# Kernel optimization log

Hardware: AMD Instinct MI355X
Metric: run time of the kernel (lower is better)

Reference implementation:

```python
import jax, jax.numpy as jnp
import numpy as np

B, CTX, QST, E, H = 8, 4096, 512, 300, 128

def setup_inputs() -> dict:
    key = jax.random.key(0)
    k1, k2, k3, k4 = jax.random.split(key, 4)
    context_sequence = jax.random.normal(k1, (B, CTX, E), dtype=jnp.float32)
    question_sequence = jax.random.normal(k2, (B, QST, E), dtype=jnp.float32)
    question_mask = jnp.ones((B, QST), dtype=jnp.int32)
    # dense layer params (PyTorch Linear: y = x @ W.T + b)
    bound = 1.0 / np.sqrt(E)
    W = jax.random.uniform(k3, (H, E), minval=-bound, maxval=bound, dtype=jnp.float32)
    b = jax.random.uniform(k4, (H,), minval=-bound, maxval=bound, dtype=jnp.float32)
    return {"context_sequence": context_sequence, "question_sequence": question_sequence,
            "question_mask": question_mask, "W": W, "b": b}

def reference(context_sequence, question_sequence, question_mask, W, b):
    # ReLU(dense(x)) for both sequences
    ctx_logits = jax.nn.relu(jnp.einsum('bce,he->bch', context_sequence, W) + b)   # [B, CTX, H]
    qst_logits = jax.nn.relu(jnp.einsum('bqe,he->bqh', question_sequence, W) + b)  # [B, QST, H]
    scores = jnp.einsum('bch,bqh->bcq', ctx_logits, qst_logits)                    # [B, CTX, QST]
    scores = jnp.where(question_mask[:, None, :] == 0, -jnp.inf, scores)
    attn = jax.nn.softmax(scores, axis=-1)
    return jnp.einsum('bcq,bqh->bch', attn, qst_logits)                            # [B, CTX, H]
```

## Files before the change

kernel.cpp:

```cpp
#include <hip/hip_runtime.h>
#include <hip/hip_bf16.h>

#define BB   8
#define SCTX 4096
#define SQ   512
#define EE   300
#define HH   128
#define EP   320
#define CST  328
#define QCH  136
#define LOG2E 1.4426950408889634f

typedef short bhalf4 __attribute__((ext_vector_type(4)));
typedef short short8 __attribute__((ext_vector_type(8)));
typedef float f32x4  __attribute__((ext_vector_type(4)));
typedef unsigned u32x4 __attribute__((ext_vector_type(4)));

#define MFMA16(a, b, c) __builtin_amdgcn_mfma_f32_16x16x32_bf16((a), (b), (c), 0, 0, 0)

__device__ __forceinline__ short f2bf(float f) {
  unsigned u = __builtin_bit_cast(unsigned, f);
  u += 0x7fffu + ((u >> 16) & 1u);
  return (short)(u >> 16);
}
__device__ __forceinline__ float bf2f(short s) {
  return __builtin_bit_cast(float, ((unsigned)(unsigned short)s) << 16);
}
__device__ __forceinline__ unsigned pack2(float a, float b) {
  return (unsigned)(unsigned short)f2bf(a) | ((unsigned)(unsigned short)f2bf(b) << 16);
}

__global__ void k_wpad(const float* __restrict__ W, short* __restrict__ wsw) {
  const int h = blockIdx.x, k = threadIdx.x;
  float v = (k < EE) ? W[h * EE + k] : 0.0f;
  const int m = h >> 4, t = h & 15, kk = k >> 5, quad = (k >> 3) & 3, j = k & 7;
  wsw[((kk * 8 + m) * 64 + quad * 16 + t) * 8 + j] = f2bf(v);
}

__global__ __launch_bounds__(256) void k_qlog(const float* __restrict__ qst,
                                              const short* __restrict__ wsw,
                                              const float* __restrict__ bias,
                                              short* __restrict__ ql,
                                              short* __restrict__ qlT) {
  const int b = blockIdx.y;
  const int m0 = blockIdx.x * 32;
  const int tid = threadIdx.x;
  const int w = tid >> 6, l = tid & 63, t = l & 15, quad = l >> 4;
  const int g = w >> 1, hf = w & 1;

  __shared__ __align__(16) short cst[32 * CST];

  const float4* cbase = (const float4*)(qst + (size_t)(b * SQ + m0) * EE);
#pragma unroll
  for (int j = 0; j < 10; ++j) {
    int i4 = tid + j * 256;
    if (i4 < 2400) {
      float4 v = cbase[i4];
      int row = i4 / 75, c4 = i4 - row * 75;
      short* dp = cst + row * CST + c4 * 4;
      dp[0] = f2bf(v.x); dp[1] = f2bf(v.y); dp[2] = f2bf(v.z); dp[3] = f2bf(v.w);
    }
  }
  for (int i = tid; i < 320; i += 256) {
    int row = i / 10, c = (i - row * 10) * 2;
    cst[row * CST + 300 + c] = 0;
    cst[row * CST + 301 + c] = 0;
  }
  __syncthreads();

  const short* arow = cst + (g * 16 + t) * CST;
  f32x4 acc[4] = {};
#pragma unroll
  for (int kk = 0; kk < 10; ++kk) {
    const int k = kk * 32 + quad * 8;
    short8 a = *(const short8*)(arow + k);
#pragma unroll
    for (int n = 0; n < 4; ++n) {
      short8 w8 = *(const short8*)(wsw + ((kk * 8 + hf * 4 + n) * 64 + l) * 8);
      acc[n] = MFMA16(a, w8, acc[n]);
    }
  }
#pragma unroll
  for (int n = 0; n < 4; ++n) {
    const int h = (hf * 4 + n) * 16 + t;
    const float bv = bias[h];
#pragma unroll
    for (int r = 0; r < 4; ++r) {
      float v = fmaxf(acc[n][r] + bv, 0.0f);
      short s16 = f2bf(v);
      const int row = m0 + g * 16 + quad * 4 + r;
      ql[((size_t)b * SQ + row) * HH + h] = s16;
      qlT[((size_t)b * HH + h) * SQ + row] = s16;
    }
  }
}

__global__ __launch_bounds__(256, 2) void k_attn(const float* __restrict__ ctx,
                                                 const short* __restrict__ wsw,
                                                 const float* __restrict__ bias,
                                                 const int* __restrict__ mask,
                                                 const short* __restrict__ ql,
                                                 const short* __restrict__ qlT,
                                                 float* __restrict__ out) {
  const int b = blockIdx.y;
  const int m0 = blockIdx.x * 64;
  const int tid = threadIdx.x;
  const int w = tid >> 6, l = tid & 63, t = l & 15, quad = l >> 4;
  const int g = w >> 1, hf = w & 1;

  __shared__ __align__(16) short uq[17408];
  __shared__ __align__(16) short uv[17408];
  __shared__ short maskh[SQ];
  short* cst = uq;
  short* qch = uq;
  short* clt = uv;
  short* vch = uv;

  const short8* qsrc = (const short8*)(ql + (size_t)b * SQ * HH);
  const short8* vsrc = (const short8*)(qlT + (size_t)b * HH * SQ);

  short8 qreg[8], vreg[8];
#pragma unroll
  for (int j = 0; j < 8; ++j) {
    int i = tid + j * 256;
    qreg[j] = qsrc[i];
    vreg[j] = vsrc[(i >> 4) * 64 + (i & 15)];
  }

  for (int i = tid; i < SQ; i += 256)
    maskh[i] = f2bf(mask[b * SQ + i] ? -8.0f : -1e30f);

  for (int i = 0; i < 2; ++i) {
    const float4* cbase = (const float4*)(ctx + ((size_t)b * SCTX + m0 + i * 32) * EE);
#pragma unroll
    for (int j = 0; j < 10; ++j) {
      int i4 = tid + j * 256;
      if (i4 < 2400) {
        float4 v = cbase[i4];
        int row = i4 / 75, c4 = i4 - row * 75;
        short* dp = cst + row * CST + c4 * 4;
        dp[0] = f2bf(v.x); dp[1] = f2bf(v.y); dp[2] = f2bf(v.z); dp[3] = f2bf(v.w);
      }
    }
    for (int k = tid; k < 320; k += 256) {
      int row = k / 10, c = (k - row * 10) * 2;
      cst[row * CST + 300 + c] = 0;
      cst[row * CST + 301 + c] = 0;
    }
    __syncthreads();
    const short* arow = cst + (g * 16 + t) * CST;
    f32x4 acc[4] = {};
#pragma unroll
    for (int kk = 0; kk < 10; ++kk) {
      const int k = kk * 32 + quad * 8;
      short8 a = *(const short8*)(arow + k);
#pragma unroll
      for (int n = 0; n < 4; ++n) {
        short8 w8 = *(const short8*)(wsw + ((kk * 8 + hf * 4 + n) * 64 + l) * 8);
        acc[n] = MFMA16(a, w8, acc[n]);
      }
    }
#pragma unroll
    for (int n = 0; n < 4; ++n) {
      const int h = (hf * 4 + n) * 16 + t;
      const float bv = bias[h];
#pragma unroll
      for (int r = 0; r < 4; ++r) {
        float v = fmaxf(acc[n][r] + bv, 0.0f);
        clt[(i * 32 + g * 16 + quad * 4 + r) * 136 + h] = f2bf(v);
      }
    }
    __syncthreads();
  }

  short8 af[4];
#pragma unroll
  for (int kk = 0; kk < 4; ++kk)
    af[kk] = *(const short8*)&clt[(w * 16 + t) * 136 + kk * 32 + quad * 8];
  __syncthreads();

#pragma unroll
  for (int j = 0; j < 8; ++j) {
    int i = tid + j * 256;
    *(short8*)&qch[(i >> 4) * QCH + (i & 15) * 8] = qreg[j];
    *(short8*)&vch[(i >> 4) * QCH + (i & 15) * 8] = vreg[j];
  }

  const int srcA = ((quad & 1) * 2) * 16 + t;
  const int srcB = srcA + 16;
  const bool hiq = quad >= 2;

  f32x4 o[8] = {};
  float rtot = 0.0f;
  for (int c = 0; c < 4; ++c) {
    __syncthreads();
    if (c < 3) {
#pragma unroll
      for (int j = 0; j < 8; ++j) {
        int i = tid + j * 256;
        qreg[j] = qsrc[(c + 1) * 2048 + i];
        vreg[j] = vsrc[(i >> 4) * 64 + (c + 1) * 16 + (i & 15)];
      }
    }
#pragma unroll
    for (int kk = 0; kk < 4; ++kk) {
      f32x4 svE = {0.f, 0.f, 0.f, 0.f}, svO = {0.f, 0.f, 0.f, 0.f};
      const short* qrE = qch + ((kk * 2) * 16 + t) * QCH;
      const short* qrO = qch + ((kk * 2 + 1) * 16 + t) * QCH;
#pragma unroll
      for (int kx = 0; kx < 4; ++kx) {
        short8 b8e = *(const short8*)(qrE + kx * 32 + quad * 8);
        short8 b8o = *(const short8*)(qrO + kx * 32 + quad * 8);
        svE = MFMA16(b8e, af[kx], svE);
        svO = MFMA16(b8o, af[kx], svO);
      }
      bhalf4 mbE = *(const bhalf4*)&maskh[c * 128 + (kk * 2) * 16 + quad * 4];
      bhalf4 mbO = *(const bhalf4*)&maskh[c * 128 + (kk * 2 + 1) * 16 + quad * 4];
      float pE[4], pO[4];
#pragma unroll
      for (int r = 0; r < 4; ++r) {
        pE[r] = exp2f((svE[r] + bf2f(mbE[r])) * LOG2E);
        pO[r] = exp2f((svO[r] + bf2f(mbO[r])) * LOG2E);
        rtot += pE[r] + pO[r];
      }
      unsigned pkE0 = pack2(pE[0], pE[1]), pkE1 = pack2(pE[2], pE[3]);
      unsigned pkO0 = pack2(pO[0], pO[1]), pkO1 = pack2(pO[2], pO[3]);
      unsigned sE0 = (unsigned)__shfl((int)pkE0, srcA), sE1 = (unsigned)__shfl((int)pkE1, srcA);
      unsigned sO0 = (unsigned)__shfl((int)pkO0, srcA), sO1 = (unsigned)__shfl((int)pkO1, srcA);
      unsigned tE0 = (unsigned)__shfl((int)pkE0, srcB), tE1 = (unsigned)__shfl((int)pkE1, srcB);
      unsigned tO0 = (unsigned)__shfl((int)pkO0, srcB), tO1 = (unsigned)__shfl((int)pkO1, srcB);
      u32x4 av;
      av[0] = hiq ? sO0 : sE0;
      av[1] = hiq ? sO1 : sE1;
      av[2] = hiq ? tO0 : tE0;
      av[3] = hiq ? tO1 : tE1;
      short8 pa = __builtin_bit_cast(short8, av);
#pragma unroll
      for (int n = 0; n < 8; ++n) {
        short8 v8 = *(const short8*)&vch[(n * 16 + t) * QCH + kk * 32 + quad * 8];
        o[n] = MFMA16(pa, v8, o[n]);
      }
    }
    __syncthreads();
    if (c < 3) {
#pragma unroll
      for (int j = 0; j < 8; ++j) {
        int i = tid + j * 256;
        *(short8*)&qch[(i >> 4) * QCH + (i & 15) * 8] = qreg[j];
        *(short8*)&vch[(i >> 4) * QCH + (i & 15) * 8] = vreg[j];
      }
    }
  }

  rtot += __shfl_xor(rtot, 16);
  rtot += __shfl_xor(rtot, 32);
  f32x4 rinv;
#pragma unroll
  for (int r = 0; r < 4; ++r) rinv[r] = 1.0f / __shfl(rtot, quad * 4 + r);
  float* obase = out + ((size_t)b * SCTX + m0 + w * 16) * HH;
#pragma unroll
  for (int n = 0; n < 8; ++n)
#pragma unroll
    for (int r = 0; r < 4; ++r)
      obase[(quad * 4 + r) * HH + n * 16 + t] = o[n][r] * rinv[r];
}

extern "C" void kernel_launch(void* const* d_in, const int* in_sizes, int n_in,
                              void* d_out, int out_size, void* d_ws, size_t ws_size,
                              hipStream_t stream) {
  const float* ctx  = (const float*)d_in[0];
  const float* qst  = (const float*)d_in[1];
  const int*   mask = (const int*)d_in[2];
  const float* W    = (const float*)d_in[3];
  const float* bias = (const float*)d_in[4];
  float* out = (float*)d_out;

  short* wsw  = (short*)d_ws;
  short* ql   = (short*)((char*)d_ws + 81920);
  short* qlT  = ql + (size_t)BB * SQ * HH;

  k_wpad<<<dim3(HH), dim3(EP), 0, stream>>>(W, wsw);
  k_qlog<<<dim3(SQ / 32, BB), dim3(256), 0, stream>>>(qst, wsw, bias, ql, qlT);
  k_attn<<<dim3(SCTX / 64, BB), dim3(256), 0, stream>>>(ctx, wsw, bias, mask, ql, qlT, out);
}
```

Baseline: 140.2 us.

## Load Q/V chunks directly into LDS with XOR-swizzled layout

Replaces the register-staged prefetch of question logits (load to registers, then store to padded LDS) with direct global-to-LDS loads via global_load_lds. The padded row stride is replaced by an XOR swizzle to avoid bank conflicts, shrinking LDS use. This frees the 16 prefetch vector registers and the LDS store instructions. In exchange it loses the overlap of the next chunk's global loads with the current chunk's compute, since each chunk is now loaded and waited on synchronously.

```diff
diff --git a/kernel.cpp b/kernel.cpp
--- a/kernel.cpp
+++ b/kernel.cpp
@@ -8,7 +8,6 @@
 #define HH   128
 #define EP   320
 #define CST  328
-#define QCH  136
 #define LOG2E 1.4426950408889634f
 
 typedef short bhalf4 __attribute__((ext_vector_type(4)));
@@ -28,6 +27,11 @@
 }
 __device__ __forceinline__ unsigned pack2(float a, float b) {
   return (unsigned)(unsigned short)f2bf(a) | ((unsigned)(unsigned short)f2bf(b) << 16);
+}
+__device__ __forceinline__ void gload16(const void* g, void* lds) {
+  __builtin_amdgcn_global_load_lds(
+      (const __attribute__((address_space(1))) void*)g,
+      (__attribute__((address_space(3))) void*)lds, 16, 0, 0);
 }
 
 __global__ void k_wpad(const float* __restrict__ W, short* __restrict__ wsw) {
@@ -108,24 +112,13 @@
   const int w = tid >> 6, l = tid & 63, t = l & 15, quad = l >> 4;
   const int g = w >> 1, hf = w & 1;
 
-  __shared__ __align__(16) short uq[17408];
-  __shared__ __align__(16) short uv[17408];
+  __shared__ __align__(16) short uq[16384];
+  __shared__ __align__(16) short uv[16384];
   __shared__ short maskh[SQ];
   short* cst = uq;
   short* qch = uq;
   short* clt = uv;
   short* vch = uv;
-
-  const short8* qsrc = (const short8*)(ql + (size_t)b * SQ * HH);
-  const short8* vsrc = (const short8*)(qlT + (size_t)b * HH * SQ);
-
-  short8 qreg[8], vreg[8];
-#pragma unroll
-  for (int j = 0; j < 8; ++j) {
-    int i = tid + j * 256;
-    qreg[j] = qsrc[i];
-    vreg[j] = vsrc[(i >> 4) * 64 + (i & 15)];
-  }
 
   for (int i = tid; i < SQ; i += 256)
     maskh[i] = f2bf(mask[b * SQ + i] ? -8.0f : -1e30f);
@@ -179,38 +172,37 @@
     af[kk] = *(const short8*)&clt[(w * 16 + t) * 136 + kk * 32 + quad * 8];
   __syncthreads();
 
-#pragma unroll
-  for (int j = 0; j < 8; ++j) {
-    int i = tid + j * 256;
-    *(short8*)&qch[(i >> 4) * QCH + (i & 15) * 8] = qreg[j];
-    *(short8*)&vch[(i >> 4) * QCH + (i & 15) * 8] = vreg[j];
-  }
-
   const int srcA = ((quad & 1) * 2) * 16 + t;
   const int srcB = srcA + 16;
   const bool hiq = quad >= 2;
+  const int sx = (t & 7) << 3;
+  const int rl = l >> 4;
+  const int cb = (l & 15) * 16;
 
   f32x4 o[8] = {};
   float rtot = 0.0f;
   for (int c = 0; c < 4; ++c) {
-    __syncthreads();
-    if (c < 3) {
-#pragma unroll
-      for (int j = 0; j < 8; ++j) {
-        int i = tid + j * 256;
-        qreg[j] = qsrc[(c + 1) * 2048 + i];
-        vreg[j] = vsrc[(i >> 4) * 64 + (c + 1) * 16 + (i & 15)];
-      }
-    }
+#pragma unroll
+    for (int s = 0; s < 8; ++s) {
+      const int row = w * 32 + s * 4 + rl;
+      const int sw = cb ^ ((row & 7) << 4);
+      gload16((const char*)(ql + ((size_t)b * SQ + c * 128 + row) * HH) + sw,
+              qch + (w * 32 + s * 4) * 128);
+      gload16((const char*)(qlT + ((size_t)b * HH + row) * SQ + c * 128) + sw,
+              vch + (w * 32 + s * 4) * 128);
+    }
+    __syncthreads();
+
 #pragma unroll
     for (int kk = 0; kk < 4; ++kk) {
       f32x4 svE = {0.f, 0.f, 0.f, 0.f}, svO = {0.f, 0.f, 0.f, 0.f};
-      const short* qrE = qch + ((kk * 2) * 16 + t) * QCH;
-      const short* qrO = qch + ((kk * 2 + 1) * 16 + t) * QCH;
+      const short* qrE = qch + ((kk * 2) * 16 + t) * 128;
+      const short* qrO = qrE + 16 * 128;
 #pragma unroll
       for (int kx = 0; kx < 4; ++kx) {
-        short8 b8e = *(const short8*)(qrE + kx * 32 + quad * 8);
-        short8 b8o = *(const short8*)(qrO + kx * 32 + quad * 8);
+        const int co = (kx * 32 + quad * 8) ^ sx;
+        short8 b8e = *(const short8*)(qrE + co);
+        short8 b8o = *(const short8*)(qrO + co);
         svE = MFMA16(b8e, af[kx], svE);
         svO = MFMA16(b8o, af[kx], svO);
       }
@@ -237,19 +229,12 @@
       short8 pa = __builtin_bit_cast(short8, av);
 #pragma unroll
       for (int n = 0; n < 8; ++n) {
-        short8 v8 = *(const short8*)&vch[(n * 16 + t) * QCH + kk * 32 + quad * 8];
+        const int co = (kk * 32 + quad * 8) ^ sx;
+        short8 v8 = *(const short8*)&vch[(n * 16 + t) * 128 + co];
         o[n] = MFMA16(pa, v8, o[n]);
       }
     }
     __syncthreads();
-    if (c < 3) {
-#pragma unroll
-      for (int j = 0; j < 8; ++j) {
-        int i = tid + j * 256;
-        *(short8*)&qch[(i >> 4) * QCH + (i & 15) * 8] = qreg[j];
-        *(short8*)&vch[(i >> 4) * QCH + (i & 15) * 8] = vreg[j];
-      }
-    }
   }
 
   rtot += __shfl_xor(rtot, 16);
```

Result: faster. 122.0 us (-13.0%).
